# Optimization experiments

Measured on AMD Instinct MI355X. Metric: run time of the kernel, lower is better.

The kernel has to match this reference:

```python
import jax, jax.numpy as jnp
import numpy as np

EMB = 512
HEADS = 8
HEAD_DIM = EMB // HEADS


def setup_inputs() -> dict:
    key = jax.random.key(0)
    ks = jax.random.split(key, 8)
    S, B = 2048, 2
    q = jax.random.normal(ks[0], (S, B, EMB), dtype=jnp.float32)
    k = jax.random.normal(ks[1], (S, B, EMB), dtype=jnp.float32)
    v = jax.random.normal(ks[2], (S, B, EMB), dtype=jnp.float32)
    sc = 1.0 / np.sqrt(HEAD_DIM)
    Wq = jax.random.normal(ks[3], (HEAD_DIM, HEAD_DIM), dtype=jnp.float32) * sc
    Wk = jax.random.normal(ks[4], (HEAD_DIM, HEAD_DIM), dtype=jnp.float32) * sc
    Wv = jax.random.normal(ks[5], (HEAD_DIM, HEAD_DIM), dtype=jnp.float32) * sc
    Wfc = jax.random.normal(ks[6], (EMB, EMB), dtype=jnp.float32) * (1.0 / np.sqrt(EMB))
    bfc = jax.random.normal(ks[7], (EMB,), dtype=jnp.float32) * 0.01
    return {"q": q, "k": k, "v": v, "Wq": Wq, "Wk": Wk, "Wv": Wv, "Wfc": Wfc, "bfc": bfc}


def reference(q, k, v, Wq, Wk, Wv, Wfc, bfc):
    query_len, batch, emb = q.shape
    key_len = k.shape[0]
    value_len = v.shape[0]
    # Faithful to the original: plain reshape (NOT transpose) from [S,B,E] -> [B,H,S,D]
    qh = q.reshape(batch, HEADS, query_len, HEAD_DIM)
    kh = k.reshape(batch, HEADS, key_len, HEAD_DIM)
    vh = v.reshape(batch, HEADS, value_len, HEAD_DIM)
    # torch Linear(head_dim, head_dim, bias=False): y = x @ W.T
    Q = qh @ Wq.T
    K = kh @ Wk.T
    V = vh @ Wv.T
    QK = jnp.einsum('bhqd,bhkd->bhqk', Q, K)  # [B,H,S,S] score matrix (memory-bound)
    filt = jax.nn.softmax(QK / np.sqrt(HEAD_DIM).astype(np.float32), axis=3)
    att = jnp.einsum('bhqk,bhkd->bhqd', filt, V)
    att = att.reshape(query_len, batch, emb)
    return att @ Wfc.T + bfc
```

## Files before the change

### kernel.cpp

```cpp
#include <hip/hip_runtime.h>
#include <hip/hip_bf16.h>


typedef __attribute__((ext_vector_type(8))) __bf16 bf16x8;
typedef __attribute__((ext_vector_type(4))) float f32x4;
typedef __attribute__((ext_vector_type(16))) float f32x16;
typedef __attribute__((ext_vector_type(4))) unsigned short u16x4;
typedef __attribute__((ext_vector_type(4))) unsigned int u32x4;
typedef unsigned short u16;
typedef unsigned int u32;

static __device__ __forceinline__ u16 f2bf(float x) {
    u32 u = __float_as_uint(x);
    u += 0x7fff + ((u >> 16) & 1);
    return (u16)(u >> 16);
}
static __device__ __forceinline__ float bf2f(u16 h) {
    return __uint_as_float(((u32)h) << 16);
}
static __device__ __forceinline__ u32 pk2(float lo, float hi) {
    __hip_bfloat162 h2 = __float22bfloat162_rn(make_float2(lo, hi));
    u32 r; __builtin_memcpy(&r, &h2, 4); return r;
}

__global__ __launch_bounds__(256) void proj_kernel(
    const float* __restrict__ q, const float* __restrict__ k, const float* __restrict__ v,
    const float* __restrict__ Wq, const float* __restrict__ Wk, const float* __restrict__ Wv,
    const float* __restrict__ Wfc,
    u16* __restrict__ Qf, u16* __restrict__ Kf, u16* __restrict__ Vf,
    u16* __restrict__ Wb, float* __restrict__ KnSq)
{
    const int mode = blockIdx.z;
    const int t = threadIdx.x;

    if (mode == 3) {
        int i = (blockIdx.x * 256 + t) * 4;
        float4 val = *(const float4*)(Wfc + i);
        uint2 b = { pk2(val.x, val.y), pk2(val.z, val.w) };
        *(uint2*)(Wb + i) = b;
        return;
    }

    const float* A = (mode == 0) ? q : (mode == 1) ? k : v;
    const float* W = (mode == 0) ? Wq : (mode == 1) ? Wk : Wv;
    const float osc = (mode == 0) ? 0.18033688011112042f : 1.0f;

    __shared__ alignas(16) u16 Ash[128 * 88];
    __shared__ alignas(16) u16 Wsh[64 * 88];
    __shared__ float red[128];

    const int m0 = blockIdx.x * 128;
    const int w = t >> 6, l = t & 63;
    const int r16 = l & 15, q4 = l >> 4;

    {
        const float4* A4 = (const float4*)(A + (size_t)m0 * 64);
        const int c4 = t & 15;
        #pragma unroll
        for (int i = 0; i < 8; ++i) {
            int row = (t >> 4) + i * 16;
            float4 val = A4[row * 16 + c4];
            uint2 bb = { pk2(val.x, val.y), pk2(val.z, val.w) };
            *(uint2*)(Ash + row * 88 + c4 * 4) = bb;
        }
        const float4* W4 = (const float4*)W;
        #pragma unroll
        for (int i = 0; i < 4; ++i) {
            int row = (t >> 4) + i * 16;
            float4 val = W4[row * 16 + c4];
            uint2 bb = { pk2(val.x, val.y), pk2(val.z, val.w) };
            *(uint2*)(Wsh + row * 88 + c4 * 4) = bb;
        }
    }
    __syncthreads();

    bf16x8 af[2][2], wf[4][2];
    #pragma unroll
    for (int mc = 0; mc < 2; ++mc)
        #pragma unroll
        for (int kk = 0; kk < 2; ++kk)
            af[mc][kk] = *(const bf16x8*)(Ash + (w * 32 + mc * 16 + r16) * 88 + kk * 32 + q4 * 8);
    #pragma unroll
    for (int nc = 0; nc < 4; ++nc)
        #pragma unroll
        for (int kk = 0; kk < 2; ++kk)
            wf[nc][kk] = *(const bf16x8*)(Wsh + (nc * 16 + r16) * 88 + kk * 32 + q4 * 8);

    f32x4 acc[2][4];
    const f32x4 zero = {0.f, 0.f, 0.f, 0.f};
    #pragma unroll
    for (int mc = 0; mc < 2; ++mc)
        #pragma unroll
        for (int nc = 0; nc < 4; ++nc) {
            acc[mc][nc] = __builtin_amdgcn_mfma_f32_16x16x32_bf16(af[mc][0], wf[nc][0], zero, 0, 0, 0);
            acc[mc][nc] = __builtin_amdgcn_mfma_f32_16x16x32_bf16(af[mc][1], wf[nc][1], acc[mc][nc], 0, 0, 0);
        }

    __syncthreads();

    const int g = m0 >> 11, t0 = (m0 & 2047) >> 6;

    if (mode < 2) {
        #pragma unroll
        for (int mc = 0; mc < 2; ++mc)
            #pragma unroll
            for (int nc = 0; nc < 4; ++nc)
                #pragma unroll
                for (int r = 0; r < 4; ++r)
                    Ash[(w * 32 + mc * 16 + q4 * 4 + r) * 72 + nc * 16 + r16] = f2bf(acc[mc][nc][r] * osc);
        __syncthreads();
        u16* Out = (mode == 0) ? Qf : Kf;
        #pragma unroll
        for (int i = 0; i < 4; ++i) {
            int idx = i * 256 + t;
            int ll = idx & 63;
            int r = idx >> 6;
            int tl = r >> 3, c2 = (r >> 2) & 1, s = r & 3;
            int row = tl * 64 + c2 * 32 + (ll & 31);
            int col = s * 16 + (ll >> 5) * 8;
            u32x4 d = *(const u32x4*)(Ash + row * 72 + col);
            *(u32x4*)(Out + ((size_t)(((g * 32 + t0 + tl) * 2 + c2) * 4 + s) * 64 + ll) * 8) = d;
        }
        if (mode == 1) {
            if (t < 128) {
                float ss = 0.f;
                #pragma unroll
                for (int c = 0; c < 8; ++c) {
                    u32x4 d = *(const u32x4*)(Ash + t * 72 + c * 8);
                    #pragma unroll
                    for (int j = 0; j < 4; ++j) {
                        float lo = bf2f((u16)(d[j] & 0xffff));
                        float hi = bf2f((u16)(d[j] >> 16));
                        ss += lo * lo + hi * hi;
                    }
                }
                red[t] = ss;
            }
            __syncthreads();
            if (t < 64) red[t] = fmaxf(red[t], red[t + 64]);
            __syncthreads();
            if (t < 32) red[t] = fmaxf(red[t], red[t + 32]);
            __syncthreads();
            if (t == 0) {
                float mx = red[0];
                for (int i = 1; i < 32; ++i) mx = fmaxf(mx, red[i]);
                KnSq[blockIdx.x] = mx;
            }
        }
    } else {
        #pragma unroll
        for (int mc = 0; mc < 2; ++mc)
            #pragma unroll
            for (int nc = 0; nc < 4; ++nc)
                #pragma unroll
                for (int r = 0; r < 4; ++r)
                    Ash[(nc * 16 + r16) * 136 + w * 32 + mc * 16 + q4 * 4 + r] = f2bf(acc[mc][nc][r]);
        __syncthreads();
        #pragma unroll
        for (int i = 0; i < 4; ++i) {
            int idx = i * 256 + t;
            int ll = idx & 63;
            int r = idx >> 6;
            int tl = r >> 3, kh = (r >> 2) & 1, dc = (r >> 1) & 1, s2 = r & 1;
            int d = dc * 32 + (ll & 31);
            int keycol = tl * 64 + kh * 32 + s2 * 16 + (ll >> 5) * 8;
            u32x4 val = *(const u32x4*)(Ash + d * 136 + keycol);
            *(u32x4*)(Vf + ((size_t)((((g * 32 + t0 + tl) * 2 + kh) * 2 + dc) * 2 + s2) * 64 + ll) * 8) = val;
        }
    }
}

__global__ __launch_bounds__(256) void flash_kernel(
    const u16* __restrict__ Qf, const u16* __restrict__ Kf,
    const u16* __restrict__ Vf, const float* __restrict__ KnSq,
    u16* __restrict__ Att)
{
    const int bi = blockIdx.x;
    const int g = bi & 15;
    const int qt = bi >> 4;
    const int t = threadIdx.x, w = t >> 6, l = t & 63;
    const int q5 = l & 31, h = l >> 5;
    const int qs = w >> 1, kh = w & 1;

    __shared__ alignas(16) unsigned char smem[26624];
    u16* const pwRow = (u16*)smem + w * 1280 + q5 * 40;

    const u16* qbase = Qf + ((size_t)(((g * 32 + qt) * 2 + qs) * 4)) * 512 + l * 8;
    const u16* kbase = Kf + ((size_t)((g * 32 * 2 + kh) * 4)) * 512 + l * 8;
    const u16* vbase = Vf + ((size_t)((g * 32 * 2 + kh) * 4)) * 512 + l * 8;

    bf16x8 qb[4];
    #pragma unroll
    for (int s = 0; s < 4; ++s) qb[s] = *(const bf16x8*)(qbase + s * 512);

    float m;
    {
        float kss = KnSq[g * 16 + (l & 15)];
        kss = fmaxf(kss, __shfl_xor(kss, 1));
        kss = fmaxf(kss, __shfl_xor(kss, 2));
        kss = fmaxf(kss, __shfl_xor(kss, 4));
        kss = fmaxf(kss, __shfl_xor(kss, 8));
        float ss = 0.f;
        #pragma unroll
        for (int s = 0; s < 4; ++s)
            #pragma unroll
            for (int j = 0; j < 8; ++j) {
                float x = (float)qb[s][j];
                ss += x * x;
            }
        ss += __shfl_xor(ss, 32);
        m = sqrtf(ss * kss) * 1.0002f;
    }

    f32x16 mC, o0, o1, ol;
    #pragma unroll
    for (int r = 0; r < 16; ++r) { mC[r] = -m; o0[r] = 0.f; o1[r] = 0.f; ol[r] = 0.f; }

    const u16 one_bf = 0x3F80;
    bf16x8 ones;
    #pragma unroll
    for (int j = 0; j < 8; ++j) ones[j] = ((const __bf16*)&one_bf)[0];

    bf16x8 ka[4], va[4], kan[4], van[4];
    #pragma unroll
    for (int s = 0; s < 4; ++s) ka[s] = *(const bf16x8*)(kbase + s * 512);
    #pragma unroll
    for (int j = 0; j < 4; ++j) va[j] = *(const bf16x8*)(vbase + j * 512);

    for (int it = 0; it < 32; ++it) {
        const size_t nx = (size_t)((it + 1) & 31) * 4096;
        #pragma unroll
        for (int s = 0; s < 4; ++s) kan[s] = *(const bf16x8*)(kbase + nx + s * 512);
        #pragma unroll
        for (int j = 0; j < 4; ++j) van[j] = *(const bf16x8*)(vbase + nx + j * 512);

        f32x16 s;
        s = __builtin_amdgcn_mfma_f32_32x32x16_bf16(ka[0], qb[0], mC, 0, 0, 0);
        s = __builtin_amdgcn_mfma_f32_32x32x16_bf16(ka[1], qb[1], s, 0, 0, 0);
        s = __builtin_amdgcn_mfma_f32_32x32x16_bf16(ka[2], qb[2], s, 0, 0, 0);
        s = __builtin_amdgcn_mfma_f32_32x32x16_bf16(ka[3], qb[3], s, 0, 0, 0);

        float p[16];
        #pragma unroll
        for (int r = 0; r < 16; ++r) p[r] = exp2f(s[r]);

        #pragma unroll
        for (int u = 0; u < 4; ++u) {
            uint2 dd = { pk2(p[4 * u + 0], p[4 * u + 1]),
                         pk2(p[4 * u + 2], p[4 * u + 3]) };
            *(uint2*)(pwRow + u * 8 + 4 * h) = dd;
        }
        bf16x8 pb0 = *(const bf16x8*)(pwRow + (0 + h) * 8);
        bf16x8 pb1 = *(const bf16x8*)(pwRow + (2 + h) * 8);

        o0 = __builtin_amdgcn_mfma_f32_32x32x16_bf16(va[0], pb0, o0, 0, 0, 0);
        o0 = __builtin_amdgcn_mfma_f32_32x32x16_bf16(va[1], pb1, o0, 0, 0, 0);
        o1 = __builtin_amdgcn_mfma_f32_32x32x16_bf16(va[2], pb0, o1, 0, 0, 0);
        o1 = __builtin_amdgcn_mfma_f32_32x32x16_bf16(va[3], pb1, o1, 0, 0, 0);
        ol = __builtin_amdgcn_mfma_f32_32x32x16_bf16(ones, pb0, ol, 0, 0, 0);
        ol = __builtin_amdgcn_mfma_f32_32x32x16_bf16(ones, pb1, ol, 0, 0, 0);

        #pragma unroll
        for (int s2 = 0; s2 < 4; ++s2) { ka[s2] = kan[s2]; va[s2] = van[s2]; }
    }

    float psq = ol[0];

    float* const Fsh = (float*)smem;
    float* const LsF = (float*)(smem + 16896);
    u16*  const Osh = (u16*)(smem + 17408);

    __syncthreads();
    if (kh == 1) {
        float* fp = Fsh + (qs * 64 + l) * 33;
        #pragma unroll
        for (int r = 0; r < 16; ++r) { fp[r] = o0[r]; fp[16 + r] = o1[r]; }
        fp[32] = psq;
        LsF[qs * 64 + l] = psq;
    }
    __syncthreads();
    if (kh == 0) {
        const float* fp = Fsh + (qs * 64 + l) * 33;
        float inv = 1.0f / (psq + LsF[qs * 64 + l]);
        const int qloc = qs * 32 + q5;
        #pragma unroll
        for (int u = 0; u < 4; ++u) {
            uint2 b0 = { pk2((o0[4*u+0] + fp[4*u+0]) * inv, (o0[4*u+1] + fp[4*u+1]) * inv),
                         pk2((o0[4*u+2] + fp[4*u+2]) * inv, (o0[4*u+3] + fp[4*u+3]) * inv) };
            *(uint2*)(Osh + qloc * 72 + 8 * u + 4 * h) = b0;
            uint2 b1 = { pk2((o1[4*u+0] + fp[16+4*u+0]) * inv, (o1[4*u+1] + fp[16+4*u+1]) * inv),
                         pk2((o1[4*u+2] + fp[16+4*u+2]) * inv, (o1[4*u+3] + fp[16+4*u+3]) * inv) };
            *(uint2*)(Osh + qloc * 72 + 32 + 8 * u + 4 * h) = b1;
        }
    }
    __syncthreads();
    {
        int row = t >> 2, cb = (t & 3) * 16;
        u16* dst = Att + ((size_t)(g * 2048 + qt * 64 + row)) * 64 + cb;
        *(u32x4*)(dst)     = *(const u32x4*)(Osh + row * 72 + cb);
        *(u32x4*)(dst + 8) = *(const u32x4*)(Osh + row * 72 + cb + 8);
    }
}

__global__ __launch_bounds__(256) void fc_kernel(
    const u16* __restrict__ Att, const u16* __restrict__ Wb,
    const float* __restrict__ bfc, float* __restrict__ out)
{
    __shared__ alignas(16) u16 Ash[2][64 * 64];
    __shared__ alignas(16) u16 Wsh[2][64 * 64];

    const int t = threadIdx.x, w = t >> 6, l = t & 63;
    const int r16 = l & 15, q4 = l >> 4;
    const int r7 = r16 & 7;
    const int m0 = blockIdx.x * 64, n0 = blockIdx.y * 64;

    const int rr = t >> 3, ck = t & 7;
    const int sw0 = (ck ^ (rr & 7)) * 8;
    const int fr0 = (q4 ^ r7) * 8;
    const int fr1 = ((q4 + 4) ^ r7) * 8;

    {
        #pragma unroll
        for (int h = 0; h < 2; ++h) {
            int row = h * 32 + rr;
            *(u32x4*)(&Ash[0][row * 64 + sw0]) = *(const u32x4*)(Att + (size_t)(m0 + row) * 512 + ck * 8);
            *(u32x4*)(&Wsh[0][row * 64 + sw0]) = *(const u32x4*)(Wb + (size_t)(n0 + row) * 512 + ck * 8);
        }
    }
    __syncthreads();

    f32x4 acc[4];
    const f32x4 zero = {0.f, 0.f, 0.f, 0.f};
    #pragma unroll
    for (int nc = 0; nc < 4; ++nc) acc[nc] = zero;

    for (int it = 0; it < 8; ++it) {
        const int cur = it & 1;
        const bool hasn = (it < 7);

        u32x4 anx[2], wnx[2];
        if (hasn) {
            #pragma unroll
            for (int h = 0; h < 2; ++h) {
                int row = h * 32 + rr;
                anx[h] = *(const u32x4*)(Att + (size_t)(m0 + row) * 512 + (it + 1) * 64 + ck * 8);
                wnx[h] = *(const u32x4*)(Wb + (size_t)(n0 + row) * 512 + (it + 1) * 64 + ck * 8);
            }
        }

        bf16x8 af[2], wf[4][2];
        af[0] = *(const bf16x8*)(&Ash[cur][(w * 16 + r16) * 64 + fr0]);
        af[1] = *(const bf16x8*)(&Ash[cur][(w * 16 + r16) * 64 + fr1]);
        #pragma unroll
        for (int nc = 0; nc < 4; ++nc) {
            wf[nc][0] = *(const bf16x8*)(&Wsh[cur][(nc * 16 + r16) * 64 + fr0]);
            wf[nc][1] = *(const bf16x8*)(&Wsh[cur][(nc * 16 + r16) * 64 + fr1]);
        }

        #pragma unroll
        for (int nc = 0; nc < 4; ++nc) {
            acc[nc] = __builtin_amdgcn_mfma_f32_16x16x32_bf16(af[0], wf[nc][0], acc[nc], 0, 0, 0);
            acc[nc] = __builtin_amdgcn_mfma_f32_16x16x32_bf16(af[1], wf[nc][1], acc[nc], 0, 0, 0);
        }

        if (hasn) {
            const int nxt = cur ^ 1;
            #pragma unroll
            for (int h = 0; h < 2; ++h) {
                int row = h * 32 + rr;
                *(u32x4*)(&Ash[nxt][row * 64 + sw0]) = anx[h];
                *(u32x4*)(&Wsh[nxt][row * 64 + sw0]) = wnx[h];
            }
        }
        __syncthreads();
    }

    #pragma unroll
    for (int nc = 0; nc < 4; ++nc) {
        float bb = bfc[n0 + nc * 16 + r16];
        #pragma unroll
        for (int r = 0; r < 4; ++r) {
            int row = m0 + w * 16 + q4 * 4 + r;
            out[(size_t)row * 512 + n0 + nc * 16 + r16] = acc[nc][r] + bb;
        }
    }
}

extern "C" void kernel_launch(void* const* d_in, const int* in_sizes, int n_in,
                              void* d_out, int out_size, void* d_ws, size_t ws_size,
                              hipStream_t stream) {
    (void)in_sizes; (void)n_in; (void)out_size; (void)ws_size;
    const float* q   = (const float*)d_in[0];
    const float* k   = (const float*)d_in[1];
    const float* v   = (const float*)d_in[2];
    const float* Wq  = (const float*)d_in[3];
    const float* Wk  = (const float*)d_in[4];
    const float* Wv  = (const float*)d_in[5];
    const float* Wfc = (const float*)d_in[6];
    const float* bfc = (const float*)d_in[7];
    float* out = (float*)d_out;

    u16* Qf = (u16*)d_ws;
    u16* Kf = Qf + 2097152;
    u16* Vf = Kf + 2097152;
    u16* At = Vf + 2097152;
    u16* Wb = At + 2097152;
    float* KnSq = (float*)((char*)d_ws + 17301504);

    proj_kernel<<<dim3(256, 1, 4), 256, 0, stream>>>(q, k, v, Wq, Wk, Wv, Wfc,
                                                     Qf, Kf, Vf, Wb, KnSq);
    flash_kernel<<<dim3(512), 256, 0, stream>>>(Qf, Kf, Vf, KnSq, At);
    fc_kernel<<<dim3(64, 8), 256, 0, stream>>>(At, Wb, bfc, out);
}
```

Before: 129.2 us.

## Split flash attention key range across four waves per query slice

The flash kernel now runs 512 threads per block, with four waves per query slice instead of two. Each wave covers a quarter of the key sequence, so the loop is 16 iterations instead of 32. The partial outputs and row sums from three waves go through a larger shared-memory buffer and are added together in wave 0 before normalisation. This shortens the serial key loop and adds wave-level parallelism. In exchange it uses more shared memory per block, which may lower occupancy, and it adds a larger reduction.

Measured after the change: 129.2 us. Within noise of the previous version (-0.1%).

```diff
diff --git a/kernel.cpp b/kernel.cpp
--- a/kernel.cpp
+++ b/kernel.cpp
@@ -170,7 +170,7 @@
     }
 }
 
-__global__ __launch_bounds__(256) void flash_kernel(
+__global__ __launch_bounds__(512) void flash_kernel(
     const u16* __restrict__ Qf, const u16* __restrict__ Kf,
     const u16* __restrict__ Vf, const float* __restrict__ KnSq,
     u16* __restrict__ Att)
@@ -180,14 +180,16 @@
     const int qt = bi >> 4;
     const int t = threadIdx.x, w = t >> 6, l = t & 63;
     const int q5 = l & 31, h = l >> 5;
-    const int qs = w >> 1, kh = w & 1;
-
-    __shared__ alignas(16) unsigned char smem[26624];
+    const int qs = w >> 2;
+    const int kq = w & 3;
+    const int kh2 = kq & 1, th = kq >> 1;
+
+    __shared__ alignas(16) unsigned char smem[61440];
     u16* const pwRow = (u16*)smem + w * 1280 + q5 * 40;
 
     const u16* qbase = Qf + ((size_t)(((g * 32 + qt) * 2 + qs) * 4)) * 512 + l * 8;
-    const u16* kbase = Kf + ((size_t)((g * 32 * 2 + kh) * 4)) * 512 + l * 8;
-    const u16* vbase = Vf + ((size_t)((g * 32 * 2 + kh) * 4)) * 512 + l * 8;
+    const u16* kbase = Kf + ((size_t)(((g * 32 + th * 16) * 2 + kh2) * 4)) * 512 + l * 8;
+    const u16* vbase = Vf + ((size_t)((((g * 32 + th * 16) * 2 + kh2) * 2) * 2)) * 512 + l * 8;
 
     bf16x8 qb[4];
     #pragma unroll
@@ -227,8 +229,8 @@
     #pragma unroll
     for (int j = 0; j < 4; ++j) va[j] = *(const bf16x8*)(vbase + j * 512);
 
-    for (int it = 0; it < 32; ++it) {
-        const size_t nx = (size_t)((it + 1) & 31) * 4096;
+    for (int it = 0; it < 16; ++it) {
+        const size_t nx = (size_t)((it + 1) & 15) * 4096;
         #pragma unroll
         for (int s = 0; s < 4; ++s) kan[s] = *(const bf16x8*)(kbase + nx + s * 512);
         #pragma unroll
@@ -267,38 +269,42 @@
     float psq = ol[0];
 
     float* const Fsh = (float*)smem;
-    float* const LsF = (float*)(smem + 16896);
-    u16*  const Osh = (u16*)(smem + 17408);
-
-    __syncthreads();
-    if (kh == 1) {
-        float* fp = Fsh + (qs * 64 + l) * 33;
+    u16*  const Osh = (u16*)(smem + 52224);
+
+    __syncthreads();
+    if (kq != 0) {
+        float* fp = Fsh + ((qs * 3) + (kq - 1)) * (64 * 34) + l * 34;
         #pragma unroll
         for (int r = 0; r < 16; ++r) { fp[r] = o0[r]; fp[16 + r] = o1[r]; }
         fp[32] = psq;
-        LsF[qs * 64 + l] = psq;
-    }
-    __syncthreads();
-    if (kh == 0) {
-        const float* fp = Fsh + (qs * 64 + l) * 33;
-        float inv = 1.0f / (psq + LsF[qs * 64 + l]);
+    }
+    __syncthreads();
+    if (kq == 0) {
+        float ltot = psq;
+        #pragma unroll
+        for (int b = 0; b < 3; ++b) {
+            const float* fp = Fsh + (qs * 3 + b) * (64 * 34) + l * 34;
+            ltot += fp[32];
+            #pragma unroll
+            for (int r = 0; r < 16; ++r) { o0[r] += fp[r]; o1[r] += fp[16 + r]; }
+        }
+        float inv = 1.0f / ltot;
         const int qloc = qs * 32 + q5;
         #pragma unroll
         for (int u = 0; u < 4; ++u) {
-            uint2 b0 = { pk2((o0[4*u+0] + fp[4*u+0]) * inv, (o0[4*u+1] + fp[4*u+1]) * inv),
-                         pk2((o0[4*u+2] + fp[4*u+2]) * inv, (o0[4*u+3] + fp[4*u+3]) * inv) };
+            uint2 b0 = { pk2(o0[4*u+0] * inv, o0[4*u+1] * inv),
+                         pk2(o0[4*u+2] * inv, o0[4*u+3] * inv) };
             *(uint2*)(Osh + qloc * 72 + 8 * u + 4 * h) = b0;
-            uint2 b1 = { pk2((o1[4*u+0] + fp[16+4*u+0]) * inv, (o1[4*u+1] + fp[16+4*u+1]) * inv),
-                         pk2((o1[4*u+2] + fp[16+4*u+2]) * inv, (o1[4*u+3] + fp[16+4*u+3]) * inv) };
+            uint2 b1 = { pk2(o1[4*u+0] * inv, o1[4*u+1] * inv),
+                         pk2(o1[4*u+2] * inv, o1[4*u+3] * inv) };
             *(uint2*)(Osh + qloc * 72 + 32 + 8 * u + 4 * h) = b1;
         }
     }
     __syncthreads();
     {
-        int row = t >> 2, cb = (t & 3) * 16;
+        int row = t >> 3, cb = (t & 7) * 8;
         u16* dst = Att + ((size_t)(g * 2048 + qt * 64 + row)) * 64 + cb;
-        *(u32x4*)(dst)     = *(const u32x4*)(Osh + row * 72 + cb);
-        *(u32x4*)(dst + 8) = *(const u32x4*)(Osh + row * 72 + cb + 8);
+        *(u32x4*)(dst) = *(const u32x4*)(Osh + row * 72 + cb);
     }
 }
 
@@ -409,6 +415,6 @@
 
     proj_kernel<<<dim3(256, 1, 4), 256, 0, stream>>>(q, k, v, Wq, Wk, Wv, Wfc,
                                                      Qf, Kf, Vf, Wb, KnSq);
-    flash_kernel<<<dim3(512), 256, 0, stream>>>(Qf, Kf, Vf, KnSq, At);
+    flash_kernel<<<dim3(512), 512, 0, stream>>>(Qf, Kf, Vf, KnSq, At);
     fc_kernel<<<dim3(64, 8), 256, 0, stream>>>(At, Wb, bfc, out);
 }
```
